# Optimization experiments

Hardware: AMD Instinct MI355X
Metric: run time of the kernel (lower is better)

Reference implementation:

```python
import jax, jax.numpy as jnp
import numpy as np

N = 100000
E = 3200000


def setup_inputs() -> dict:
    key = jax.random.key(0)
    ks = jax.random.split(key, 8)
    x = jax.random.normal(ks[0], (N,), dtype=jnp.float32)
    edge_index = jax.random.randint(ks[1], (2, E), 0, N, dtype=jnp.int32)
    W_in = jax.random.normal(ks[2], (1, 32), dtype=jnp.float32) * 0.5
    b_in = jnp.zeros((32,), dtype=jnp.float32)
    W_mid = jax.random.normal(ks[3], (32, 32), dtype=jnp.float32) * (1.0 / np.sqrt(32))
    b_mid = jnp.zeros((32,), dtype=jnp.float32)
    W_out = jax.random.normal(ks[4], (32, 1), dtype=jnp.float32) * (1.0 / np.sqrt(32))
    b_out = jnp.zeros((1,), dtype=jnp.float32)
    return {"x": x, "edge_index": edge_index, "W_in": W_in, "b_in": b_in,
            "W_mid": W_mid, "b_mid": b_mid, "W_out": W_out, "b_out": b_out}


def _gcn_layer(h, src, dst, norm, W, b, n_nodes):
    # linear transform first (out_dim <= in_dim keeps message traffic small)
    h = h @ W                              # [N, out]
    msg = h[src] * norm[:, None]           # gather + edge-normalize, [E+N, out]
    out = jax.ops.segment_sum(msg, dst, num_segments=n_nodes)  # scatter-add
    return out + b


def reference(x, edge_index, W_in, b_in, W_mid, b_mid, W_out, b_out):
    n = x.shape[0]
    # add_self_loops
    loops = jnp.arange(n, dtype=edge_index.dtype)
    src = jnp.concatenate([edge_index[0], loops])
    dst = jnp.concatenate([edge_index[1], loops])
    # symmetric degree normalization (GCN): deg over target nodes incl. self loops
    deg = jax.ops.segment_sum(jnp.ones_like(src, dtype=x.dtype), dst, num_segments=n)
    dinv = jnp.where(deg > 0, jax.lax.rsqrt(deg), 0.0)
    norm = dinv[src] * dinv[dst]           # [E+N]

    h = x[:, None]                         # view(-1, 1)
    h = jax.nn.relu(_gcn_layer(h, src, dst, norm, W_in, b_in, n))
    h = jax.nn.relu(_gcn_layer(h, src, dst, norm, W_mid, b_mid, n))
    h = jax.nn.relu(_gcn_layer(h, src, dst, norm, W_mid, b_mid, n))  # conv_mid reused (shared weights)
    h = _gcn_layer(h, src, dst, norm, W_out, b_out, n)
    return jax.nn.sigmoid(h)               # [N, 1]
```

## Files before the change

kernel.cpp:

```cpp
#include <hip/hip_runtime.h>
#include <math.h>


#define BLK 256
#define PBLK 1024
#define BBLK 512
#define NBLK 256
#define MAXCHUNK 12544
#define CAP 5120

#define FP8_SCALE 64.0f
#define FP8_INV   0.015625f

typedef float f32x2 __attribute__((ext_vector_type(2)));


__global__ void k_initcur(int* __restrict__ cursor, int NB,
                          int* __restrict__ ph1, int* __restrict__ ph2) {
    int b = blockIdx.x * blockDim.x + threadIdx.x;
    if (b < NB) cursor[b] = b * CAP;
    if (b < 8) { ph1[b] = 0; ph2[b] = 0; }
}

__global__ void __launch_bounds__(PBLK) k_place(
        const int* __restrict__ src, const int* __restrict__ dst,
        int* __restrict__ cursor, int* __restrict__ bkt, int E, int chunk) {
    __shared__ int hist[788];
    __shared__ int lofs[788];
    __shared__ int lcur[788];
    __shared__ int tmp[PBLK];
    __shared__ int stage[MAXCHUNK];
    int t = threadIdx.x;
    int b0 = blockIdx.x * chunk;
    int b1 = min(E, b0 + chunk);
    int n = b1 - b0;
    if (t < 788) hist[t] = 0;
    __syncthreads();
    for (int k = b0 + t; k < b1; k += PBLK) atomicAdd(&hist[dst[k] >> 7], 1);
    __syncthreads();
    int v = (t < 788) ? hist[t] : 0;
    tmp[t] = v;
    __syncthreads();
    for (int o = 1; o < PBLK; o <<= 1) {
        int a = (t >= o) ? tmp[t - o] : 0;
        __syncthreads();
        tmp[t] += a;
        __syncthreads();
    }
    int ex = tmp[t] - v;
    if (t < 788) { lofs[t] = ex; lcur[t] = ex; }
    __syncthreads();
    if (t < 782) {
        int c = hist[t];
        hist[t] = c ? atomicAdd(&cursor[t], c) : 0;
    }
    __syncthreads();
    for (int k = b0 + t; k < b1; k += PBLK) {
        int d = dst[k], s = src[k];
        int b = d >> 7;
        int p = atomicAdd(&lcur[b], 1);
        stage[p] = s | ((d & 127) << 17);
    }
    __syncthreads();
    for (int k = t; k < n; k += PBLK) {
        int lo = 0, hi = 781;
        while (lo < hi) {
            int mid = (lo + hi + 1) >> 1;
            if (lofs[mid] <= k) lo = mid; else hi = mid - 1;
        }
        int pos = hist[lo] + (k - lofs[lo]);
        if (pos < (lo + 1) * CAP) bkt[pos] = stage[k];
    }
}

__global__ void __launch_bounds__(BBLK) k_build(
        const int* __restrict__ cursor, const int* __restrict__ bkt,
        const float* __restrict__ x,
        uint2* __restrict__ rs2, int* __restrict__ ss,
        float* __restrict__ dinv, float* __restrict__ sa, int N) {
    __shared__ int cnt[1024], lofs[1024], lcur[1024];
    __shared__ int tmp[BBLK];
    __shared__ int stg[CAP];
    int b = blockIdx.x, t = threadIdx.x;
    int node_base = b << 7;
    int gb = b * CAP;
    int sz = min(cursor[b] - gb, CAP);
    for (int i = t; i < 1024; i += BBLK) cnt[i] = 0;
    __syncthreads();
    const int* q = bkt + gb;
    for (int k = t; k < sz; k += BBLK) {
        int v = q[k];
        int bin = (((v >> 17) & 127) << 3) | ((v & 0x1FFFF) >> 14);
        atomicAdd(&cnt[bin], 1);
    }
    __syncthreads();
    int vals[2];
    int sum = 0;
    int i0 = t << 1;
    #pragma unroll
    for (int r = 0; r < 2; ++r) { vals[r] = cnt[i0 + r]; sum += vals[r]; }
    tmp[t] = sum;
    __syncthreads();
    for (int o = 1; o < BBLK; o <<= 1) {
        int a = (t >= o) ? tmp[t - o] : 0;
        __syncthreads();
        tmp[t] += a;
        __syncthreads();
    }
    int run = tmp[t] - sum;
    #pragma unroll
    for (int r = 0; r < 2; ++r) {
        int c = vals[r];
        lofs[i0 + r] = run;
        lcur[i0 + r] = run;
        run += c;
    }
    __syncthreads();
    if (t < 128) {
        int i = node_base + t;
        if (i < N) {
            int beg = lofs[t << 3];
            int end = (t < 127) ? lofs[(t + 1) << 3] : sz;
            int len = end - beg;
            rs2[i] = make_uint2((unsigned)(gb + beg), (unsigned)len);
            float d = rsqrtf((float)len + 1.0f);
            dinv[i] = d;
            sa[i] = x[i] * d;
        }
    }
    __syncthreads();
    for (int k = t; k < sz; k += BBLK) {
        int v = q[k];
        int bin = (((v >> 17) & 127) << 3) | ((v & 0x1FFFF) >> 14);
        int pos = atomicAdd(&lcur[bin], 1);
        stg[pos] = v & 0x1FFFF;
    }
    __syncthreads();
    for (int k = t; k < sz; k += BBLK) ss[gb + k] = stg[k];
}


__global__ void k_l1aggG(const uint2* __restrict__ rs2, const int* __restrict__ ss,
                         const float* __restrict__ sa, const float* __restrict__ dinv,
                         const float* __restrict__ Win, const float* __restrict__ bin,
                         const float* __restrict__ Wmid, unsigned char* __restrict__ Gh,
                         int N) {
    int t = blockIdx.x * blockDim.x + threadIdx.x;
    int i = t >> 5, l = t & 31;
    if (i >= N) return;
    float wcol[32];
    #pragma unroll
    for (int k = 0; k < 32; ++k) wcol[k] = Wmid[k * 32 + l];
    uint2 r = rs2[i];
    int beg = (int)r.x, end = (int)(r.x + r.y);
    float s = 0.f;
    for (int e = beg + l; e < end; e += 32) s += sa[ss[e]];
    #pragma unroll
    for (int m = 16; m; m >>= 1) s += __shfl_xor(s, m, 32);
    float d = dinv[i];
    float h = d * (s + sa[i]);
    float F = h * Win[l] + bin[l];
    F = F > 0.f ? F : 0.f;
    float g = 0.f;
    #pragma unroll
    for (int k = 0; k < 32; ++k) g += __shfl(F, k, 32) * wcol[k];
    float v = g * d * FP8_SCALE;
    Gh[t] = (unsigned char)(__builtin_amdgcn_cvt_pk_fp8_f32(v, v, 0, false) & 0xFF);
}

__device__ __forceinline__ void acc_row(f32x2* a2, uint2 v) {
    a2[0] += __builtin_amdgcn_cvt_pk_f32_fp8(v.x, false);
    a2[1] += __builtin_amdgcn_cvt_pk_f32_fp8(v.x, true);
    a2[2] += __builtin_amdgcn_cvt_pk_f32_fp8(v.y, false);
    a2[3] += __builtin_amdgcn_cvt_pk_f32_fp8(v.y, true);
}

__global__ void __launch_bounds__(256) k_agg2mv(
        const uint2* __restrict__ rs2, const int* __restrict__ ss,
        const uint2* __restrict__ G8, const float* __restrict__ dinv,
        const float* __restrict__ b, const float* __restrict__ Wmid,
        unsigned char* __restrict__ Gh3, int N) {
    __shared__ float sW[1024];
    __shared__ float sF[8][33];
    __shared__ float sdv[8];
    int t = threadIdx.x;
    #pragma unroll
    for (int r = 0; r < 4; ++r) sW[r * 256 + t] = Wmid[r * 256 + t];
    int tg = blockIdx.x * blockDim.x + t;
    int g = tg >> 5;
    int lane = t & 31, sub = lane >> 2, fl = lane & 3;
    int grp = t >> 5;
    bool act = (g < N);
    f32x2 a2[4];
    #pragma unroll
    for (int j = 0; j < 4; ++j) a2[j] = (f32x2)0.f;
    if (act) {
        uint2 r = rs2[g];
        int beg = (int)r.x;
        int end = beg + (int)r.y;
        int idx[8];
        #pragma unroll
        for (int rr = 0; rr < 8; ++rr) {
            int slot = beg + sub + 8 * rr;
            int ssv = ss[slot];
            idx[rr] = (slot < end) ? ssv : N;
        }
        uint2 v[8];
        #pragma unroll
        for (int rr = 0; rr < 8; ++rr) v[rr] = G8[(long long)idx[rr] * 4 + fl];
        #pragma unroll
        for (int rr = 0; rr < 8; ++rr) acc_row(a2, v[rr]);
        if (sub == 0) acc_row(a2, G8[(long long)g * 4 + fl]);
        for (int e = beg + 64 + sub; e < end; e += 8)
            acc_row(a2, G8[(long long)ss[e] * 4 + fl]);
    }
    float acc[8];
    #pragma unroll
    for (int j = 0; j < 8; ++j) acc[j] = a2[j >> 1][j & 1];
    #pragma unroll
    for (int j = 0; j < 8; ++j) {
        acc[j] += __shfl_xor(acc[j], 4);
        acc[j] += __shfl_xor(acc[j], 8);
        acc[j] += __shfl_xor(acc[j], 16);
    }
    if (act && sub == 0) {
        float d = dinv[g];
        if (fl == 0) sdv[grp] = d;
        float ds = d * FP8_INV;
        #pragma unroll
        for (int j = 0; j < 8; ++j) {
            float v = ds * acc[j] + b[fl * 8 + j];
            sF[grp][fl * 8 + j] = v > 0.f ? v : 0.f;
        }
    }
    __syncthreads();
    if (act) {
        float s = 0.f;
        #pragma unroll
        for (int k = 0; k < 32; ++k) s += sF[grp][k] * sW[k * 32 + lane];
        float v = s * sdv[grp] * FP8_SCALE;
        Gh3[(long long)g * 32 + lane] =
            (unsigned char)(__builtin_amdgcn_cvt_pk_fp8_f32(v, v, 0, false) & 0xFF);
    }
}

__global__ void __launch_bounds__(256) k_agg3(
        const uint2* __restrict__ rs2, const int* __restrict__ ss,
        const uint2* __restrict__ G8, const float* __restrict__ dinv,
        const float* __restrict__ b, const float* __restrict__ Wout,
        float* __restrict__ sa, int N) {
    int t = blockIdx.x * blockDim.x + threadIdx.x;
    int g = t >> 5;
    if (g >= N) return;
    int lane = t & 31, sub = lane >> 2, fl = lane & 3;
    uint2 r = rs2[g];
    int beg = (int)r.x;
    int end = beg + (int)r.y;
    f32x2 a2[4];
    #pragma unroll
    for (int j = 0; j < 4; ++j) a2[j] = (f32x2)0.f;
    int idx[8];
    #pragma unroll
    for (int rr = 0; rr < 8; ++rr) {
        int slot = beg + sub + 8 * rr;
        int ssv = ss[slot];
        idx[rr] = (slot < end) ? ssv : N;
    }
    uint2 v[8];
    #pragma unroll
    for (int rr = 0; rr < 8; ++rr) v[rr] = G8[(long long)idx[rr] * 4 + fl];
    #pragma unroll
    for (int rr = 0; rr < 8; ++rr) acc_row(a2, v[rr]);
    if (sub == 0) acc_row(a2, G8[(long long)g * 4 + fl]);
    for (int e = beg + 64 + sub; e < end; e += 8)
        acc_row(a2, G8[(long long)ss[e] * 4 + fl]);
    float acc[8];
    #pragma unroll
    for (int j = 0; j < 8; ++j) acc[j] = a2[j >> 1][j & 1];
    #pragma unroll
    for (int j = 0; j < 8; ++j) {
        acc[j] += __shfl_xor(acc[j], 4);
        acc[j] += __shfl_xor(acc[j], 8);
        acc[j] += __shfl_xor(acc[j], 16);
    }
    if (sub == 0) {
        float d = dinv[g];
        float ds = d * FP8_INV;
        float p = 0.f;
        #pragma unroll
        for (int j = 0; j < 8; ++j) {
            float v = ds * acc[j] + b[fl * 8 + j];
            v = v > 0.f ? v : 0.f;
            p += v * Wout[fl * 8 + j];
        }
        p += __shfl_xor(p, 1, 32);
        p += __shfl_xor(p, 2, 32);
        if (fl == 0) sa[g] = p * d;
    }
}

__global__ void k_final_agg(const uint2* __restrict__ rs2, const int* __restrict__ ss,
                            const float* __restrict__ sa, const float* __restrict__ dinv,
                            const float* __restrict__ bout, float* __restrict__ out, int N) {
    int t = blockIdx.x * blockDim.x + threadIdx.x;
    int i = t >> 5, l = t & 31;
    if (i >= N) return;
    uint2 r = rs2[i];
    int beg = (int)r.x, end = (int)(r.x + r.y);
    float s = 0.f;
    for (int e = beg + l; e < end; e += 32) s += sa[ss[e]];
    #pragma unroll
    for (int m = 16; m; m >>= 1) s += __shfl_xor(s, m, 32);
    if (l == 0) {
        float z = dinv[i] * (s + sa[i]) + bout[0];
        out[i] = 1.0f / (1.0f + expf(-z));
    }
}

extern "C" void kernel_launch(void* const* d_in, const int* in_sizes, int n_in,
                              void* d_out, int out_size, void* d_ws, size_t ws_size,
                              hipStream_t stream) {
    const float* x    = (const float*)d_in[0];
    const int*   ei   = (const int*)  d_in[1];
    const float* Win  = (const float*)d_in[2];
    const float* bin  = (const float*)d_in[3];
    const float* Wmid = (const float*)d_in[4];
    const float* bmid = (const float*)d_in[5];
    const float* Wout = (const float*)d_in[6];
    const float* bout = (const float*)d_in[7];
    float* out = (float*)d_out;

    int N = in_sizes[0];
    int E = in_sizes[1] / 2;
    const int* src = ei;
    const int* dst = ei + E;

    int NB = (N + 127) >> 7;
    int chunk = (E + NBLK - 1) / NBLK;

    int* cursor = (int*)d_ws;
    uint2* rs2  = (uint2*)(cursor + 1024);
    int* ss     = (int*)(rs2 + N + 8);
    float* dinv = (float*)(ss + (size_t)NB * CAP + 64);
    float* sa   = dinv + N;
    unsigned char* Gh  = (unsigned char*)(sa + N);
    unsigned char* Gh3 = Gh + 32 * (size_t)N + 32;
    int* bkt    = (int*)(Gh3 + 32 * (size_t)N + 32);

    int NT   = N * 32;
    int gN32 = (NT + BLK - 1) / BLK;

    k_initcur<<<(NB + BLK - 1) / BLK, BLK, 0, stream>>>(
        cursor, NB, (int*)(Gh + 32 * (size_t)N), (int*)(Gh3 + 32 * (size_t)N));
    k_place<<<NBLK, PBLK, 0, stream>>>(src, dst, cursor, bkt, E, chunk);
    k_build<<<NB, BBLK, 0, stream>>>(cursor, bkt, x, rs2, ss, dinv, sa, N);

    k_l1aggG<<<gN32, BLK, 0, stream>>>(rs2, ss, sa, dinv, Win, bin, Wmid, Gh, N);

    k_agg2mv<<<gN32, BLK, 0, stream>>>(rs2, ss, (const uint2*)Gh, dinv, bmid,
                                       Wmid, Gh3, N);

    k_agg3<<<gN32, BLK, 0, stream>>>(rs2, ss, (const uint2*)Gh3, dinv, bmid,
                                     Wout, sa, N);

    k_final_agg<<<gN32, BLK, 0, stream>>>(rs2, ss, sa, dinv, bout, out, N);
}
```

Measured before the change: 227.6 us.

## Pad CSR rows to multiples of eight and bucket nodes by degree class

The CSR build now pads each node's neighbor list to a multiple of 8 using a sentinel index N. It also counts nodes per degree class (ceil(len/8), capped at 8) and builds a node permutation list with a scan and a ballot-based fill. The layer-2 and layer-3 aggregation kernels walk that list, so warps process nodes of the same degree class, and they call a specialized gather with a compile-time unroll matching the class. This removes per-slot bounds masking and wasted gathers for low-degree nodes and reduces divergence. In exchange it adds two small kernels, more shared memory and scans in k_build, and larger ss storage, and the permuted node order scatters the output writes.

Measured after the change: 318.9 us. 40.1% more time.

```diff
diff --git a/kernel.cpp b/kernel.cpp
--- a/kernel.cpp
+++ b/kernel.cpp
@@ -7,7 +7,9 @@
 #define BBLK 512
 #define NBLK 256
 #define MAXCHUNK 12544
-#define CAP 5120
+#define BCAP 5120
+#define SCAP 6144
+#define SZCLAMP 5120
 
 #define FP8_SCALE 64.0f
 #define FP8_INV   0.015625f
@@ -15,10 +17,11 @@
 typedef float f32x2 __attribute__((ext_vector_type(2)));
 
 
-__global__ void k_initcur(int* __restrict__ cursor, int NB,
+__global__ void k_initcur(int* __restrict__ cursor, int NB, int* __restrict__ gcnt,
                           int* __restrict__ ph1, int* __restrict__ ph2) {
     int b = blockIdx.x * blockDim.x + threadIdx.x;
-    if (b < NB) cursor[b] = b * CAP;
+    if (b < NB) cursor[b] = b * BCAP;
+    if (b < 9) gcnt[b] = 0;
     if (b < 8) { ph1[b] = 0; ph2[b] = 0; }
 }
 
@@ -69,7 +72,7 @@
             if (lofs[mid] <= k) lo = mid; else hi = mid - 1;
         }
         int pos = hist[lo] + (k - lofs[lo]);
-        if (pos < (lo + 1) * CAP) bkt[pos] = stage[k];
+        if (pos < (lo + 1) * BCAP) bkt[pos] = stage[k];
     }
 }
 
@@ -77,15 +80,20 @@
         const int* __restrict__ cursor, const int* __restrict__ bkt,
         const float* __restrict__ x,
         uint2* __restrict__ rs2, int* __restrict__ ss,
-        float* __restrict__ dinv, float* __restrict__ sa, int N) {
+        float* __restrict__ dinv, float* __restrict__ sa,
+        int* __restrict__ gcnt, int N) {
     __shared__ int cnt[1024], lofs[1024], lcur[1024];
     __shared__ int tmp[BBLK];
-    __shared__ int stg[CAP];
+    __shared__ int stg[SCAP];
+    __shared__ int pB[128], pL[128];
+    __shared__ int ccnt[9];
     int b = blockIdx.x, t = threadIdx.x;
     int node_base = b << 7;
-    int gb = b * CAP;
-    int sz = min(cursor[b] - gb, CAP);
+    int gb = b * BCAP;
+    int gbs = b * SCAP;
+    int sz = min(cursor[b] - gb, SZCLAMP);
     for (int i = t; i < 1024; i += BBLK) cnt[i] = 0;
+    if (t < 9) ccnt[t] = 0;
     __syncthreads();
     const int* q = bkt + gb;
     for (int k = t; k < sz; k += BBLK) {
@@ -116,17 +124,44 @@
         run += c;
     }
     __syncthreads();
+    int len = 0, padl = 0;
     if (t < 128) {
         int i = node_base + t;
         if (i < N) {
             int beg = lofs[t << 3];
             int end = (t < 127) ? lofs[(t + 1) << 3] : sz;
-            int len = end - beg;
-            rs2[i] = make_uint2((unsigned)(gb + beg), (unsigned)len);
+            len = end - beg;
+        }
+        padl = (len + 7) & ~7;
+    }
+    tmp[t] = (t < 128) ? padl : 0;
+    __syncthreads();
+    for (int o = 1; o < 128; o <<= 1) {
+        int a = (t >= o && t < 128) ? tmp[t - o] : 0;
+        __syncthreads();
+        if (t < 128) tmp[t] += a;
+        __syncthreads();
+    }
+    if (t < 128) {
+        int pbeg = tmp[t] - padl;
+        pB[t] = pbeg;
+        pL[t] = len;
+        int i = node_base + t;
+        if (i < N) {
+            rs2[i] = make_uint2((unsigned)(gbs + pbeg), (unsigned)len);
             float d = rsqrtf((float)len + 1.0f);
             dinv[i] = d;
             sa[i] = x[i] * d;
-        }
+            int c = min((len + 7) >> 3, 8);
+            atomicAdd(&ccnt[c], 1);
+        }
+    }
+    __syncthreads();
+    int szp = tmp[127];
+    if (t < 9 && ccnt[t]) atomicAdd(&gcnt[t], ccnt[t]);
+    for (int i = t; i < 1024; i += BBLK) {
+        int nn = i >> 3;
+        lcur[i] = pB[nn] + (lofs[i] - lofs[nn << 3]);
     }
     __syncthreads();
     for (int k = t; k < sz; k += BBLK) {
@@ -136,7 +171,41 @@
         stg[pos] = v & 0x1FFFF;
     }
     __syncthreads();
-    for (int k = t; k < sz; k += BBLK) ss[gb + k] = stg[k];
+    if (t < 128) {
+        int pbeg = pB[t];
+        int l2 = pL[t];
+        int p2 = (l2 + 7) & ~7;
+        for (int k = l2; k < p2; ++k) stg[pbeg + k] = N;
+    }
+    __syncthreads();
+    for (int k = t; k < szp; k += BBLK) ss[gbs + k] = stg[k];
+}
+
+__global__ void k_cscan(const int* __restrict__ gcnt, int* __restrict__ gcur) {
+    if (threadIdx.x == 0) {
+        int s = 0;
+        for (int c = 0; c < 9; ++c) { gcur[c] = s; s += gcnt[c]; }
+    }
+}
+
+__global__ void k_cfill(const uint2* __restrict__ rs2, int* __restrict__ gcur,
+                        int* __restrict__ list, int N) {
+    int i = blockIdx.x * blockDim.x + threadIdx.x;
+    int lane = threadIdx.x & 63;
+    int cls = 9;
+    if (i < N) cls = min(((int)rs2[i].y + 7) >> 3, 8);
+    for (int c = 0; c < 9; ++c) {
+        unsigned long long m = __ballot(cls == c);
+        if (m == 0ull) continue;
+        if (cls == c) {
+            int ldr = (int)(__ffsll((long long)m) - 1);
+            int rank = __popcll(m & ((1ull << lane) - 1ull));
+            int base = 0;
+            if (lane == ldr) base = atomicAdd(&gcur[c], (int)__popcll(m));
+            base = __shfl(base, ldr, 64);
+            list[base + rank] = i;
+        }
+    }
 }
 
 
@@ -175,11 +244,55 @@
     a2[3] += __builtin_amdgcn_cvt_pk_f32_fp8(v.y, true);
 }
 
+template<int D>
+__device__ __forceinline__ void gatherD(const unsigned char* __restrict__ Gb,
+                                        const int* __restrict__ ss,
+                                        int sbeg, int fo, f32x2* a2) {
+    int idx[D];
+    #pragma unroll
+    for (int rr = 0; rr < D; ++rr) idx[rr] = ss[sbeg + 8 * rr];
+    uint2 v[D];
+    #pragma unroll
+    for (int rr = 0; rr < D; ++rr)
+        v[rr] = *(const uint2*)(Gb + (((unsigned)idx[rr]) << 5) + fo);
+    #pragma unroll
+    for (int rr = 0; rr < D; ++rr) acc_row(a2, v[rr]);
+}
+
+__device__ __forceinline__ void gather_cls(const unsigned char* __restrict__ Gb,
+                                           const int* __restrict__ ss,
+                                           int beg, int sub, int fo, int len,
+                                           f32x2* a2) {
+    int cls = (len + 7) >> 3;
+    int c = min(cls, 8);
+    int sbeg = beg + sub;
+    switch (c) {
+        case 1: gatherD<1>(Gb, ss, sbeg, fo, a2); break;
+        case 2: gatherD<2>(Gb, ss, sbeg, fo, a2); break;
+        case 3: gatherD<3>(Gb, ss, sbeg, fo, a2); break;
+        case 4: gatherD<4>(Gb, ss, sbeg, fo, a2); break;
+        case 5: gatherD<5>(Gb, ss, sbeg, fo, a2); break;
+        case 6: gatherD<6>(Gb, ss, sbeg, fo, a2); break;
+        case 7: gatherD<7>(Gb, ss, sbeg, fo, a2); break;
+        case 8: {
+            gatherD<8>(Gb, ss, sbeg, fo, a2);
+            int hi = beg + 8 * cls;
+            for (int e = sbeg + 64; e < hi; e += 8) {
+                int ix = ss[e];
+                uint2 vv = *(const uint2*)(Gb + (((unsigned)ix) << 5) + fo);
+                acc_row(a2, vv);
+            }
+            break;
+        }
+        default: break;
+    }
+}
+
 __global__ void __launch_bounds__(256) k_agg2mv(
         const uint2* __restrict__ rs2, const int* __restrict__ ss,
-        const uint2* __restrict__ G8, const float* __restrict__ dinv,
+        const unsigned char* __restrict__ Gb, const float* __restrict__ dinv,
         const float* __restrict__ b, const float* __restrict__ Wmid,
-        unsigned char* __restrict__ Gh3, int N) {
+        unsigned char* __restrict__ Gh3, const int* __restrict__ list, int N) {
     __shared__ float sW[1024];
     __shared__ float sF[8][33];
     __shared__ float sdv[8];
@@ -187,32 +300,20 @@
     #pragma unroll
     for (int r = 0; r < 4; ++r) sW[r * 256 + t] = Wmid[r * 256 + t];
     int tg = blockIdx.x * blockDim.x + t;
-    int g = tg >> 5;
+    int gi = tg >> 5;
     int lane = t & 31, sub = lane >> 2, fl = lane & 3;
     int grp = t >> 5;
-    bool act = (g < N);
+    bool act = (gi < N);
+    int g = act ? list[gi] : 0;
+    int fo = fl << 3;
     f32x2 a2[4];
     #pragma unroll
     for (int j = 0; j < 4; ++j) a2[j] = (f32x2)0.f;
     if (act) {
         uint2 r = rs2[g];
-        int beg = (int)r.x;
-        int end = beg + (int)r.y;
-        int idx[8];
-        #pragma unroll
-        for (int rr = 0; rr < 8; ++rr) {
-            int slot = beg + sub + 8 * rr;
-            int ssv = ss[slot];
-            idx[rr] = (slot < end) ? ssv : N;
-        }
-        uint2 v[8];
-        #pragma unroll
-        for (int rr = 0; rr < 8; ++rr) v[rr] = G8[(long long)idx[rr] * 4 + fl];
-        #pragma unroll
-        for (int rr = 0; rr < 8; ++rr) acc_row(a2, v[rr]);
-        if (sub == 0) acc_row(a2, G8[(long long)g * 4 + fl]);
-        for (int e = beg + 64 + sub; e < end; e += 8)
-            acc_row(a2, G8[(long long)ss[e] * 4 + fl]);
+        gather_cls(Gb, ss, (int)r.x, sub, fo, (int)r.y, a2);
+        if (sub == 0)
+            acc_row(a2, *(const uint2*)(Gb + (((unsigned)g) << 5) + fo));
     }
     float acc[8];
     #pragma unroll
@@ -246,34 +347,22 @@
 
 __global__ void __launch_bounds__(256) k_agg3(
         const uint2* __restrict__ rs2, const int* __restrict__ ss,
-        const uint2* __restrict__ G8, const float* __restrict__ dinv,
+        const unsigned char* __restrict__ Gb, const float* __restrict__ dinv,
         const float* __restrict__ b, const float* __restrict__ Wout,
-        float* __restrict__ sa, int N) {
+        float* __restrict__ sa, const int* __restrict__ list, int N) {
     int t = blockIdx.x * blockDim.x + threadIdx.x;
-    int g = t >> 5;
-    if (g >= N) return;
+    int gi = t >> 5;
+    if (gi >= N) return;
+    int g = list[gi];
     int lane = t & 31, sub = lane >> 2, fl = lane & 3;
+    int fo = fl << 3;
     uint2 r = rs2[g];
-    int beg = (int)r.x;
-    int end = beg + (int)r.y;
     f32x2 a2[4];
     #pragma unroll
     for (int j = 0; j < 4; ++j) a2[j] = (f32x2)0.f;
-    int idx[8];
-    #pragma unroll
-    for (int rr = 0; rr < 8; ++rr) {
-        int slot = beg + sub + 8 * rr;
-        int ssv = ss[slot];
-        idx[rr] = (slot < end) ? ssv : N;
-    }
-    uint2 v[8];
-    #pragma unroll
-    for (int rr = 0; rr < 8; ++rr) v[rr] = G8[(long long)idx[rr] * 4 + fl];
-    #pragma unroll
-    for (int rr = 0; rr < 8; ++rr) acc_row(a2, v[rr]);
-    if (sub == 0) acc_row(a2, G8[(long long)g * 4 + fl]);
-    for (int e = beg + 64 + sub; e < end; e += 8)
-        acc_row(a2, G8[(long long)ss[e] * 4 + fl]);
+    gather_cls(Gb, ss, (int)r.x, sub, fo, (int)r.y, a2);
+    if (sub == 0)
+        acc_row(a2, *(const uint2*)(Gb + (((unsigned)g) << 5) + fo));
     float acc[8];
     #pragma unroll
     for (int j = 0; j < 8; ++j) acc[j] = a2[j >> 1][j & 1];
@@ -339,9 +428,12 @@
     int chunk = (E + NBLK - 1) / NBLK;
 
     int* cursor = (int*)d_ws;
-    uint2* rs2  = (uint2*)(cursor + 1024);
+    int* gcnt   = cursor + 1024;
+    int* gcur   = gcnt + 16;
+    int* list   = gcur + 16;
+    uint2* rs2  = (uint2*)(list + N);
     int* ss     = (int*)(rs2 + N + 8);
-    float* dinv = (float*)(ss + (size_t)NB * CAP + 64);
+    float* dinv = (float*)(ss + (size_t)NB * SCAP + 64);
     float* sa   = dinv + N;
     unsigned char* Gh  = (unsigned char*)(sa + N);
     unsigned char* Gh3 = Gh + 32 * (size_t)N + 32;
@@ -351,17 +443,19 @@
     int gN32 = (NT + BLK - 1) / BLK;
 
     k_initcur<<<(NB + BLK - 1) / BLK, BLK, 0, stream>>>(
-        cursor, NB, (int*)(Gh + 32 * (size_t)N), (int*)(Gh3 + 32 * (size_t)N));
+        cursor, NB, gcnt, (int*)(Gh + 32 * (size_t)N), (int*)(Gh3 + 32 * (size_t)N));
     k_place<<<NBLK, PBLK, 0, stream>>>(src, dst, cursor, bkt, E, chunk);
-    k_build<<<NB, BBLK, 0, stream>>>(cursor, bkt, x, rs2, ss, dinv, sa, N);
+    k_build<<<NB, BBLK, 0, stream>>>(cursor, bkt, x, rs2, ss, dinv, sa, gcnt, N);
+    k_cscan<<<1, 64, 0, stream>>>(gcnt, gcur);
+    k_cfill<<<(N + 255) / 256, 256, 0, stream>>>(rs2, gcur, list, N);
 
     k_l1aggG<<<gN32, BLK, 0, stream>>>(rs2, ss, sa, dinv, Win, bin, Wmid, Gh, N);
 
-    k_agg2mv<<<gN32, BLK, 0, stream>>>(rs2, ss, (const uint2*)Gh, dinv, bmid,
-                                       Wmid, Gh3, N);
-
-    k_agg3<<<gN32, BLK, 0, stream>>>(rs2, ss, (const uint2*)Gh3, dinv, bmid,
-                                     Wout, sa, N);
+    k_agg2mv<<<gN32, BLK, 0, stream>>>(rs2, ss, Gh, dinv, bmid, Wmid, Gh3,
+                                       list, N);
+
+    k_agg3<<<gN32, BLK, 0, stream>>>(rs2, ss, Gh3, dinv, bmid, Wout, sa,
+                                     list, N);
 
     k_final_agg<<<gN32, BLK, 0, stream>>>(rs2, ss, sa, dinv, bout, out, N);
 }
```
